# Kernel tuning notes

Measured on AMD Instinct MI355X. Metric: run time of the kernel, lower is better.

## Reference

```python
import jax, jax.numpy as jnp
import numpy as np
import math

B, CIN, CH, H, W = 4, 64, 32, 64, 64
M_CH, DEPTH, K = 4, 3, 8
NPF = CIN // 2  # num_pos_feats per axis; pos channels = 2*NPF = CIN
TEMPERATURE = 10000.0


def sine_pos(h, w, npf, temperature=TEMPERATURE):
    # PositionEmbeddingSine with normalize=False; cumsum of ones == arange(1, n+1)
    y_embed = jnp.arange(1, h + 1, dtype=jnp.float32)
    x_embed = jnp.arange(1, w + 1, dtype=jnp.float32)
    dim_t = jnp.arange(npf, dtype=jnp.float32)
    dim_t = temperature ** (2.0 * jnp.floor(dim_t / 2.0) / npf)
    pos_x = jnp.broadcast_to(x_embed[None, :, None] / dim_t, (h, w, npf))
    pos_y = jnp.broadcast_to(y_embed[:, None, None] / dim_t, (h, w, npf))

    def interleave(p):
        return jnp.stack([jnp.sin(p[..., 0::2]), jnp.cos(p[..., 1::2])], axis=-1).reshape(h, w, npf)

    pos = jnp.concatenate([interleave(pos_y), interleave(pos_x)], axis=-1)  # (h,w,2*npf)
    return jnp.transpose(pos, (2, 0, 1))  # (2*npf, h, w)


def conv2d(x, wgt, bias, pad):
    y = jax.lax.conv_general_dilated(
        x, wgt, window_strides=(1, 1), padding=[(pad, pad), (pad, pad)],
        dimension_numbers=('NCHW', 'OIHW', 'NCHW'))
    return y + bias[None, :, None, None]


def setup_inputs() -> dict:
    key = jax.random.key(0)
    ks = jax.random.split(key, 13)
    s = 0.05
    return {
        'f':    jax.random.normal(ks[0], (B, CH, H, W), jnp.float32),
        'map':  jax.random.normal(ks[1], (B, 1, 32, 32), jnp.float32),
        'f_q':  jax.random.normal(ks[2], (B, CIN, H, W), jnp.float32),
        'f_k':  jax.random.normal(ks[3], (B, CIN, H, W), jnp.float32),
        'm_k':  jax.random.normal(ks[4], (B, 1, 32, 32), jnp.float32),
        'wq':   jax.random.normal(ks[5], (M_CH, CIN), jnp.float32) * s,
        'wk':   jax.random.normal(ks[6], (M_CH, CIN), jnp.float32) * s,
        'w_in':  jax.random.normal(ks[7], (CH, CH, 1, 1), jnp.float32) * s,
        'b_in':  jax.random.normal(ks[8], (CH,), jnp.float32) * s,
        'w_mid': jax.random.normal(ks[9], (DEPTH, CH, CH, 3, 3), jnp.float32) * s,
        'b_mid': jax.random.normal(ks[10], (DEPTH, CH), jnp.float32) * s,
        'w_out': jax.random.normal(ks[11], (1, CH, 3, 3), jnp.float32) * s,
        'b_out': jax.random.normal(ks[12], (1,), jnp.float32) * s,
    }


def reference(f, map, f_q, f_k, m_k, wq, wk, w_in, b_in, w_mid, b_mid, w_out, b_out):
    b, c, h, w = f_q.shape
    hf, wf = f.shape[2], f.shape[3]
    # self.ret: bilinear resize to f's spatial size (align_corners=False)
    map_r = jax.image.resize(map, (b, 1, hf, wf), method='bilinear')
    m_k_r = jax.image.resize(m_k, (b, 1, hf, wf), method='bilinear')

    pos = sine_pos(h, w, NPF)[None]  # (1, CIN, h, w); same for pos_emb_h/pos_emb_l
    fq_emb = f_q + pos
    fk_emb = f_k + pos

    # 1x1 convs == channel matmuls
    query = jnp.einsum('mc,bchw->bhwm', wq, fq_emb).reshape(b, h * w, M_CH)  # (b, N, m)
    key_t = jnp.einsum('mc,bchw->bmhw', wk, fk_emb).reshape(b, M_CH, h * w)  # (b, m, N)

    sim = jnp.einsum('bqm,bmk->bqk', query, key_t)   # (b, N, N)
    sim = jax.nn.softmax(sim, axis=-2)                # softmax over query axis (dim=-2)

    value = (jnp.exp(m_k_r) / math.e).reshape(b, 1, h * w)  # broadcast over query axis
    context = sim * value
    context_k, _ = jax.lax.top_k(context, K)          # (b, N, K) over last (key) axis
    context_m = jnp.mean(context_k, axis=-1)          # (b, N)
    corrected_map = context_m.reshape(b, 1, h, w)

    corrected_map = corrected_map * map_r + map_r
    rmap = 1.0 - jax.nn.sigmoid(corrected_map)

    x = rmap * f  # broadcast over channel dim
    x = conv2d(x, w_in, b_in, 0)
    for i in range(DEPTH):
        x = jax.nn.relu(conv2d(x, w_mid[i], b_mid[i], 1))
    out = conv2d(x, w_out, b_out, 1) + corrected_map
    return (x, out, corrected_map)
```

## Files before the change

### kernel.cpp

```cpp
#include <hip/hip_runtime.h>
#include <hip/hip_bf16.h>
#include <math.h>

#define BB 4
#define CIN 64
#define CH 32
#define HH 64
#define WW 64
#define NN 4096
#define MCH 4
#define NQCH 32
#define LOG2E 1.4426950408889634f
#define L2_10K 13.287712379549449f

#define Q4_OFF     1024
#define K4_OFF     66560
#define CV_OFF     132096
#define RMAP_OFF   148480
#define CMAPF_OFF  164864
#define T8_OFF     181248
#define CPSUM_OFF  181248
#define XA_OFF     181248
#define XB_OFF     705536

#define OUT_X_OFF   0
#define OUT_O_OFF   524288
#define OUT_CM_OFF  540672

#define CE(x, y) { float ce_lo = fminf(x, y); y = fmaxf(x, y); x = ce_lo; }

__device__ __forceinline__ float bilin32(const float* src, int b, int y, int x) {
    float sy = 0.5f * y - 0.25f;
    float sx = 0.5f * x - 0.25f;
    float fy0 = floorf(sy), fx0 = floorf(sx);
    int y0 = (int)fy0, x0 = (int)fx0;
    float fy = sy - fy0, fx = sx - fx0;
    int y0c = min(max(y0, 0), 31), y1c = min(max(y0 + 1, 0), 31);
    int x0c = min(max(x0, 0), 31), x1c = min(max(x0 + 1, 0), 31);
    const float* p = src + b * 1024;
    float v00 = p[y0c * 32 + x0c], v01 = p[y0c * 32 + x1c];
    float v10 = p[y1c * 32 + x0c], v11 = p[y1c * 32 + x1c];
    float v0 = v00 + fx * (v01 - v00);
    float v1 = v10 + fx * (v11 - v10);
    return v0 + fy * (v1 - v0);
}

__global__ __launch_bounds__(512) void k1_qk(
        const float* __restrict__ fq, const float* __restrict__ fk,
        const float* __restrict__ wq, const float* __restrict__ wk,
        float* __restrict__ Q4, float* __restrict__ K4) {
    __shared__ float wqs[256], wks[256];
    __shared__ float pp[1024];
    __shared__ float red[512][9];
    int tid = threadIdx.x;
    if (tid < 256) { wqs[tid] = wq[tid]; wks[tid] = wk[tid]; }
    __syncthreads();

    if (tid < 64) {
        float coord = (float)(tid + 1);
        float qy[4] = {0,0,0,0}, qx[4] = {0,0,0,0}, ky[4] = {0,0,0,0}, kx[4] = {0,0,0,0};
        for (int c = 0; c < 32; ++c) {
            float e = (2.0f * (float)(c >> 1)) * (1.0f / 32.0f);
            float ang = coord * exp2f(-e * L2_10K);
            float pr = (c & 1) ? cosf(ang) : sinf(ang);
            #pragma unroll
            for (int m = 0; m < 4; ++m) {
                qy[m] += wqs[m * 64 + c] * pr;
                qx[m] += wqs[m * 64 + 32 + c] * pr;
                ky[m] += wks[m * 64 + c] * pr;
                kx[m] += wks[m * 64 + 32 + c] * pr;
            }
        }
        #pragma unroll
        for (int m = 0; m < 4; ++m) {
            pp[0 * 256 + m * 64 + tid] = qy[m];
            pp[1 * 256 + m * 64 + tid] = qx[m];
            pp[2 * 256 + m * 64 + tid] = ky[m];
            pp[3 * 256 + m * 64 + tid] = kx[m];
        }
    }

    int qi = tid & 63, g = tid >> 6;
    int gid = blockIdx.x * 64 + qi;
    int b = gid >> 12, hw = gid & 4095;
    const float* fqb = fq + (size_t)b * CIN * NN + hw;
    const float* fkb = fk + (size_t)b * CIN * NN + hw;
    float aq[4] = {0,0,0,0}, ak[4] = {0,0,0,0};
    int c0 = g * 8;
    #pragma unroll
    for (int c = c0; c < c0 + 8; ++c) {
        float vq = fqb[c * NN];
        float vk = fkb[c * NN];
        #pragma unroll
        for (int m = 0; m < 4; ++m) {
            aq[m] += wqs[m * 64 + c] * vq;
            ak[m] += wks[m * 64 + c] * vk;
        }
    }
    #pragma unroll
    for (int m = 0; m < 4; ++m) { red[tid][m] = aq[m]; red[tid][4 + m] = ak[m]; }
    __syncthreads();
    if (tid < 64) {
        int y = hw >> 6, x = hw & 63;
        float q4[4], k4[4];
        #pragma unroll
        for (int m = 0; m < 4; ++m) {
            float sq = 0.0f, sk = 0.0f;
            #pragma unroll
            for (int j = 0; j < 8; ++j) {
                sq += red[tid + 64 * j][m];
                sk += red[tid + 64 * j][4 + m];
            }
            q4[m] = LOG2E * (sq + pp[0 * 256 + m * 64 + y] + pp[1 * 256 + m * 64 + x]);
            k4[m] = sk + pp[2 * 256 + m * 64 + y] + pp[3 * 256 + m * 64 + x];
        }
        ((float4*)Q4)[gid] = make_float4(q4[0], q4[1], q4[2], q4[3]);
        ((float4*)K4)[gid] = make_float4(k4[0], k4[1], k4[2], k4[3]);
    }
}

__global__ void k2a_colstats(const float* __restrict__ Q4, const float* __restrict__ K4,
                             float* __restrict__ cpsum) {
    int blk = blockIdx.x;
    int kblk = blk & 7;   blk >>= 3;
    int qch  = blk & 31;  blk >>= 5;
    int b    = blk;
    int tid = threadIdx.x;
    const float4* Qg = (const float4*)Q4 + b * NN + qch * 128;
    int k0 = kblk * 512 + tid;
    float4 kva = ((const float4*)K4)[b * NN + k0];
    float4 kvb = ((const float4*)K4)[b * NN + k0 + 256];
    float sa = 0.0f, sb = 0.0f;
    #pragma unroll 8
    for (int i = 0; i < 128; ++i) {
        float4 q = Qg[i];
        float da = fmaf(q.x, kva.x, fmaf(q.y, kva.y, fmaf(q.z, kva.z, q.w * kva.w)));
        float db = fmaf(q.x, kvb.x, fmaf(q.y, kvb.y, fmaf(q.z, kvb.z, q.w * kvb.w)));
        sa += exp2f(da);
        sb += exp2f(db);
    }
    cpsum[(b * NQCH + qch) * NN + k0] = sa;
    cpsum[(b * NQCH + qch) * NN + k0 + 256] = sb;
}

__global__ void k2b_cmerge(const float* __restrict__ cpsum,
                           const float* __restrict__ m_k, float* __restrict__ cvals) {
    int gid = blockIdx.x * 256 + threadIdx.x;
    int b = gid >> 12, k = gid & 4095;
    float S = 0.0f;
    #pragma unroll
    for (int j = 0; j < NQCH; ++j) S += cpsum[(b * NQCH + j) * NN + k];
    float mk = bilin32(m_k, b, k >> 6, k & 63);
    cvals[gid] = LOG2E * (mk - 1.0f) - log2f(S);
}

__global__ __launch_bounds__(256) void k3a_scan(
        const float* __restrict__ Q4, const float* __restrict__ K4,
        const float* __restrict__ cvals, float* __restrict__ t8) {
    int blk = blockIdx.x;
    int kc = blk & 15;  blk >>= 4;
    int g4 = blk & 15;  blk >>= 4;
    int b  = blk;
    int tid = threadIdx.x;
    int wave = tid >> 6, lane = tid & 63;
    int qrow = (g4 * 4 + wave) * 64 + lane;
    float4 qv = ((const float4*)Q4)[b * NN + qrow];
    const float4* Kb = (const float4*)K4 + b * NN + kc * 256;
    const float* cb = cvals + b * NN + kc * 256;

    float t0=-1e30f,t1=-1e30f,t2=-1e30f,t3=-1e30f;
    float t4=-1e30f,t5=-1e30f,t6=-1e30f,t7=-1e30f;

    #pragma unroll 2
    for (int i0 = 0; i0 < 256; i0 += 8) {
        float4 k0 = Kb[i0 + 0]; float4 k1 = Kb[i0 + 1];
        float4 k2 = Kb[i0 + 2]; float4 k3 = Kb[i0 + 3];
        float4 k4 = Kb[i0 + 4]; float4 k5 = Kb[i0 + 5];
        float4 k6 = Kb[i0 + 6]; float4 k7 = Kb[i0 + 7];
        float s0 = fmaf(qv.x,k0.x, fmaf(qv.y,k0.y, fmaf(qv.z,k0.z, qv.w*k0.w))) + cb[i0+0];
        float s1 = fmaf(qv.x,k1.x, fmaf(qv.y,k1.y, fmaf(qv.z,k1.z, qv.w*k1.w))) + cb[i0+1];
        float s2 = fmaf(qv.x,k2.x, fmaf(qv.y,k2.y, fmaf(qv.z,k2.z, qv.w*k2.w))) + cb[i0+2];
        float s3 = fmaf(qv.x,k3.x, fmaf(qv.y,k3.y, fmaf(qv.z,k3.z, qv.w*k3.w))) + cb[i0+3];
        float s4 = fmaf(qv.x,k4.x, fmaf(qv.y,k4.y, fmaf(qv.z,k4.z, qv.w*k4.w))) + cb[i0+4];
        float s5 = fmaf(qv.x,k5.x, fmaf(qv.y,k5.y, fmaf(qv.z,k5.z, qv.w*k5.w))) + cb[i0+5];
        float s6 = fmaf(qv.x,k6.x, fmaf(qv.y,k6.y, fmaf(qv.z,k6.z, qv.w*k6.w))) + cb[i0+6];
        float s7 = fmaf(qv.x,k7.x, fmaf(qv.y,k7.y, fmaf(qv.z,k7.z, qv.w*k7.w))) + cb[i0+7];
        float bm = fmaxf(fmaxf(fmaxf(s0,s1), fmaxf(s2,s3)),
                         fmaxf(fmaxf(s4,s5), fmaxf(s6,s7)));
        if (bm > t0) {
            CE(s0,s1); CE(s2,s3); CE(s4,s5); CE(s6,s7);
            CE(s0,s2); CE(s1,s3); CE(s4,s6); CE(s5,s7);
            CE(s1,s2); CE(s5,s6);
            CE(s0,s4); CE(s1,s5); CE(s2,s6); CE(s3,s7);
            CE(s2,s4); CE(s3,s5);
            CE(s1,s2); CE(s3,s4); CE(s5,s6);
            t0 = fmaxf(t0, s7); t1 = fmaxf(t1, s6); t2 = fmaxf(t2, s5); t3 = fmaxf(t3, s4);
            t4 = fmaxf(t4, s3); t5 = fmaxf(t5, s2); t6 = fmaxf(t6, s1); t7 = fmaxf(t7, s0);
            CE(t0,t4); CE(t1,t5); CE(t2,t6); CE(t3,t7);
            CE(t0,t2); CE(t1,t3); CE(t4,t6); CE(t5,t7);
            CE(t0,t1); CE(t2,t3); CE(t4,t5); CE(t6,t7);
        }
    }
    float* o = t8 + ((size_t)(b * NN + qrow)) * 128 + kc * 8;
    o[0] = t0; o[1] = t1; o[2] = t2; o[3] = t3;
    o[4] = t4; o[5] = t5; o[6] = t6; o[7] = t7;
}

__global__ void k3b_merge(const float* __restrict__ t8, const float* __restrict__ mapin,
                          float* __restrict__ rmap, float* __restrict__ cmapf,
                          float* __restrict__ outp) {
    int tid = threadIdx.x;
    int qid = blockIdx.x * 4 + (tid >> 6);
    int lane = tid & 63;
    float va = t8[(size_t)qid * 128 + lane];
    float vb = t8[(size_t)qid * 128 + 64 + lane];
    float hi = fmaxf(va, vb), lo = fminf(va, vb);
    float sm = 0.0f;
    #pragma unroll
    for (int r = 0; r < 8; ++r) {
        float m = hi;
        int ln = lane;
        #pragma unroll
        for (int off = 32; off >= 1; off >>= 1) {
            float om = __shfl_xor(m, off);
            int ol = __shfl_xor(ln, off);
            if (om > m || (om == m && ol < ln)) { m = om; ln = ol; }
        }
        sm += exp2f(m);
        if (lane == ln) { hi = lo; lo = -1e30f; }
    }
    if (lane == 0) {
        float cmv = sm * 0.125f;
        int b = qid >> 12, hw = qid & 4095;
        float mr = bilin32(mapin, b, hw >> 6, hw & 63);
        float cm = cmv * mr + mr;
        float rm = 1.0f / (1.0f + __expf(cm));
        rmap[qid] = rm;
        cmapf[qid] = cm;
        outp[OUT_CM_OFF + qid] = cm;
    }
}

__global__ void k4_conv1(const float* __restrict__ f, const float* __restrict__ rmap,
                         const float* __restrict__ w_in, const float* __restrict__ b_in,
                         float* __restrict__ xout) {
    __shared__ float ws_[1024];
    __shared__ float bs[32];
    int tid = threadIdx.x;
    for (int i = tid; i < 1024; i += 256) ws_[i] = w_in[i];
    if (tid < 32) bs[tid] = b_in[tid];
    __syncthreads();
    int gid = blockIdx.x * 256 + tid;
    int hw = gid & 4095;
    int og = (gid >> 12) & 7;
    int b  = gid >> 15;
    float rm = rmap[b * NN + hw];
    float acc[4];
    #pragma unroll
    for (int j = 0; j < 4; ++j) acc[j] = bs[og * 4 + j];
    const float* fb = f + (size_t)b * CH * NN + hw;
    for (int i = 0; i < 32; ++i) {
        float v = fb[i * NN] * rm;
        #pragma unroll
        for (int j = 0; j < 4; ++j) acc[j] += ws_[(og * 4 + j) * 32 + i] * v;
    }
    float* xo = xout + (size_t)b * CH * NN + (og * 4) * NN + hw;
    #pragma unroll
    for (int j = 0; j < 4; ++j) xo[j * NN] = acc[j];
}

__global__ void k5_conv3(const float* __restrict__ xin, const float* __restrict__ w,
                         const float* __restrict__ bias, float* __restrict__ xout,
                         float* __restrict__ outx) {
    __shared__ float tile[32][324];
    __shared__ float wsm[1152];
    __shared__ float bsm[4];
    int blk = blockIdx.x;
    int og = blk & 7;  blk >>= 3;
    int tx = blk & 3;  blk >>= 2;
    int ty = blk & 3;  blk >>= 2;
    int b  = blk;
    int tid = threadIdx.x;
    for (int i = tid; i < 1152; i += 256) wsm[i] = w[og * 1152 + i];
    if (tid < 4) bsm[tid] = bias[og * 4 + tid];
    int y0 = ty * 16 - 1, x0 = tx * 16 - 1;
    for (int i = tid; i < 32 * 324; i += 256) {
        int c = i / 324, r = i % 324;
        int yy = r / 18, xx = r % 18;
        int gy = y0 + yy, gx = x0 + xx;
        float v = 0.0f;
        if (gy >= 0 && gy < 64 && gx >= 0 && gx < 64)
            v = xin[((size_t)b * CH + c) * NN + gy * 64 + gx];
        tile[c][r] = v;
    }
    __syncthreads();
    int py = tid >> 4, px = tid & 15;
    float acc[4];
    #pragma unroll
    for (int j = 0; j < 4; ++j) acc[j] = bsm[j];
    for (int i = 0; i < 32; ++i) {
        const float* tr = &tile[i][py * 18 + px];
        float v00 = tr[0],  v01 = tr[1],  v02 = tr[2];
        float v10 = tr[18], v11 = tr[19], v12 = tr[20];
        float v20 = tr[36], v21 = tr[37], v22 = tr[38];
        #pragma unroll
        for (int j = 0; j < 4; ++j) {
            const float* wj = &wsm[j * 288 + i * 9];
            acc[j] += v00 * wj[0] + v01 * wj[1] + v02 * wj[2]
                    + v10 * wj[3] + v11 * wj[4] + v12 * wj[5]
                    + v20 * wj[6] + v21 * wj[7] + v22 * wj[8];
        }
    }
    size_t base = (size_t)b * CH * NN + (size_t)(og * 4) * NN
                + (ty * 16 + py) * 64 + tx * 16 + px;
    #pragma unroll
    for (int j = 0; j < 4; ++j) {
        float r_ = fmaxf(acc[j], 0.0f);
        xout[base + j * NN] = r_;
        if (outx) outx[base + j * NN] = r_;
    }
}

__global__ void k6_convout(const float* __restrict__ xin, const float* __restrict__ w_out,
                           const float* __restrict__ b_out, const float* __restrict__ cmapf,
                           float* __restrict__ outp) {
    __shared__ float wsm[288];
    __shared__ float red[256];
    int tid = threadIdx.x;
    for (int i = tid; i < 288; i += 256) wsm[i] = w_out[i];
    int pxi = tid & 63, g = tid >> 6;
    int gid = blockIdx.x * 64 + pxi;
    int b = gid >> 12, hw = gid & 4095;
    int y = hw >> 6, x = hw & 63;
    __syncthreads();
    float acc = 0.0f;
    int c0 = g * 8;
    for (int i = c0; i < c0 + 8; ++i) {
        const float* xi = xin + ((size_t)b * CH + i) * NN;
        #pragma unroll
        for (int ky = 0; ky < 3; ++ky) {
            int gy = y + ky - 1;
            if (gy < 0 || gy > 63) continue;
            #pragma unroll
            for (int kx = 0; kx < 3; ++kx) {
                int gx = x + kx - 1;
                if (gx < 0 || gx > 63) continue;
                acc += xi[gy * 64 + gx] * wsm[i * 9 + ky * 3 + kx];
            }
        }
    }
    red[tid] = acc;
    __syncthreads();
    if (tid < 64) {
        float a = red[tid] + red[tid + 64] + red[tid + 128] + red[tid + 192]
                + b_out[0] + cmapf[gid];
        outp[OUT_O_OFF + gid] = a;
    }
}

extern "C" void kernel_launch(void* const* d_in, const int* in_sizes, int n_in,
                              void* d_out, int out_size, void* d_ws, size_t ws_size,
                              hipStream_t stream) {
    const float* f     = (const float*)d_in[0];
    const float* mapin = (const float*)d_in[1];
    const float* f_q   = (const float*)d_in[2];
    const float* f_k   = (const float*)d_in[3];
    const float* m_k   = (const float*)d_in[4];
    const float* wq    = (const float*)d_in[5];
    const float* wk    = (const float*)d_in[6];
    const float* w_in  = (const float*)d_in[7];
    const float* b_in  = (const float*)d_in[8];
    const float* w_mid = (const float*)d_in[9];
    const float* b_mid = (const float*)d_in[10];
    const float* w_out = (const float*)d_in[11];
    const float* b_out = (const float*)d_in[12];
    float* outp = (float*)d_out;
    float* ws = (float*)d_ws;

    float* Q4    = ws + Q4_OFF;
    float* K4    = ws + K4_OFF;
    float* CV    = ws + CV_OFF;
    float* CPSUM = ws + CPSUM_OFF;
    float* RMAP  = ws + RMAP_OFF;
    float* CMAPF = ws + CMAPF_OFF;
    float* T8    = ws + T8_OFF;
    float* XA    = ws + XA_OFF;
    float* XB    = ws + XB_OFF;

    k1_qk<<<256, 512, 0, stream>>>(f_q, f_k, wq, wk, Q4, K4);
    k2a_colstats<<<BB * NQCH * 8, 256, 0, stream>>>(Q4, K4, CPSUM);
    k2b_cmerge<<<64, 256, 0, stream>>>(CPSUM, m_k, CV);
    k3a_scan<<<BB * 16 * 16, 256, 0, stream>>>(Q4, K4, CV, T8);
    k3b_merge<<<BB * NN / 4, 256, 0, stream>>>(T8, mapin, RMAP, CMAPF, outp);
    k4_conv1<<<512, 256, 0, stream>>>(f, RMAP, w_in, b_in, XA);
    k5_conv3<<<512, 256, 0, stream>>>(XA, w_mid + 0 * 9216, b_mid + 0 * 32, XB, (float*)0);
    k5_conv3<<<512, 256, 0, stream>>>(XB, w_mid + 1 * 9216, b_mid + 1 * 32, XA, (float*)0);
    k5_conv3<<<512, 256, 0, stream>>>(XA, w_mid + 2 * 9216, b_mid + 2 * 32, XB, outp + OUT_X_OFF);
    k6_convout<<<256, 256, 0, stream>>>(XB, w_out, b_out, CMAPF, outp);
}
```

Before: 206.4 us.

## Double parallelism in qk projection, colstats and top-k scan kernels

Three attention kernels get finer work splits. k1 now processes 32 queries per block with 16 channel groups over 512 blocks. k2a gives each thread one key instead of two across twice as many blocks. k3a uses 512-thread blocks in which two wave groups each scan half of the 256-key chunk and merge their top-8 lists through shared memory. The aim is more waves in flight to hide latency on a GPU with many CUs, at the cost of extra reduction work, a block barrier and LDS traffic.

```diff
diff --git a/kernel.cpp b/kernel.cpp
--- a/kernel.cpp
+++ b/kernel.cpp
@@ -80,15 +80,15 @@
         }
     }
 
-    int qi = tid & 63, g = tid >> 6;
-    int gid = blockIdx.x * 64 + qi;
+    int qi = tid & 31, g = tid >> 5;
+    int gid = blockIdx.x * 32 + qi;
     int b = gid >> 12, hw = gid & 4095;
     const float* fqb = fq + (size_t)b * CIN * NN + hw;
     const float* fkb = fk + (size_t)b * CIN * NN + hw;
     float aq[4] = {0,0,0,0}, ak[4] = {0,0,0,0};
-    int c0 = g * 8;
-    #pragma unroll
-    for (int c = c0; c < c0 + 8; ++c) {
+    int c0 = g * 4;
+    #pragma unroll
+    for (int c = c0; c < c0 + 4; ++c) {
         float vq = fqb[c * NN];
         float vk = fkb[c * NN];
         #pragma unroll
@@ -100,16 +100,16 @@
     #pragma unroll
     for (int m = 0; m < 4; ++m) { red[tid][m] = aq[m]; red[tid][4 + m] = ak[m]; }
     __syncthreads();
-    if (tid < 64) {
+    if (tid < 32) {
         int y = hw >> 6, x = hw & 63;
         float q4[4], k4[4];
         #pragma unroll
         for (int m = 0; m < 4; ++m) {
             float sq = 0.0f, sk = 0.0f;
             #pragma unroll
-            for (int j = 0; j < 8; ++j) {
-                sq += red[tid + 64 * j][m];
-                sk += red[tid + 64 * j][4 + m];
+            for (int j = 0; j < 16; ++j) {
+                sq += red[tid + 32 * j][m];
+                sk += red[tid + 32 * j][4 + m];
             }
             q4[m] = LOG2E * (sq + pp[0 * 256 + m * 64 + y] + pp[1 * 256 + m * 64 + x]);
             k4[m] = sk + pp[2 * 256 + m * 64 + y] + pp[3 * 256 + m * 64 + x];
@@ -119,28 +119,25 @@
     }
 }
 
-__global__ void k2a_colstats(const float* __restrict__ Q4, const float* __restrict__ K4,
-                             float* __restrict__ cpsum) {
+__global__ __launch_bounds__(256) void k2a_colstats(
+        const float* __restrict__ Q4, const float* __restrict__ K4,
+        float* __restrict__ cpsum) {
     int blk = blockIdx.x;
-    int kblk = blk & 7;   blk >>= 3;
+    int kblk = blk & 15;  blk >>= 4;
     int qch  = blk & 31;  blk >>= 5;
     int b    = blk;
     int tid = threadIdx.x;
     const float4* Qg = (const float4*)Q4 + b * NN + qch * 128;
-    int k0 = kblk * 512 + tid;
-    float4 kva = ((const float4*)K4)[b * NN + k0];
-    float4 kvb = ((const float4*)K4)[b * NN + k0 + 256];
-    float sa = 0.0f, sb = 0.0f;
+    int k0 = kblk * 256 + tid;
+    float4 kv = ((const float4*)K4)[b * NN + k0];
+    float s = 0.0f;
     #pragma unroll 8
     for (int i = 0; i < 128; ++i) {
         float4 q = Qg[i];
-        float da = fmaf(q.x, kva.x, fmaf(q.y, kva.y, fmaf(q.z, kva.z, q.w * kva.w)));
-        float db = fmaf(q.x, kvb.x, fmaf(q.y, kvb.y, fmaf(q.z, kvb.z, q.w * kvb.w)));
-        sa += exp2f(da);
-        sb += exp2f(db);
-    }
-    cpsum[(b * NQCH + qch) * NN + k0] = sa;
-    cpsum[(b * NQCH + qch) * NN + k0 + 256] = sb;
+        float d = fmaf(q.x, kv.x, fmaf(q.y, kv.y, fmaf(q.z, kv.z, q.w * kv.w)));
+        s += exp2f(d);
+    }
+    cpsum[(b * NQCH + qch) * NN + k0] = s;
 }
 
 __global__ void k2b_cmerge(const float* __restrict__ cpsum,
@@ -154,25 +151,27 @@
     cvals[gid] = LOG2E * (mk - 1.0f) - log2f(S);
 }
 
-__global__ __launch_bounds__(256) void k3a_scan(
+__global__ __launch_bounds__(512) void k3a_scan(
         const float* __restrict__ Q4, const float* __restrict__ K4,
         const float* __restrict__ cvals, float* __restrict__ t8) {
+    __shared__ float sbuf[4][64][9];
     int blk = blockIdx.x;
     int kc = blk & 15;  blk >>= 4;
     int g4 = blk & 15;  blk >>= 4;
     int b  = blk;
     int tid = threadIdx.x;
     int wave = tid >> 6, lane = tid & 63;
-    int qrow = (g4 * 4 + wave) * 64 + lane;
+    int wsub = wave & 3, half = wave >> 2;
+    int qrow = (g4 * 4 + wsub) * 64 + lane;
     float4 qv = ((const float4*)Q4)[b * NN + qrow];
-    const float4* Kb = (const float4*)K4 + b * NN + kc * 256;
-    const float* cb = cvals + b * NN + kc * 256;
+    const float4* Kb = (const float4*)K4 + b * NN + kc * 256 + half * 128;
+    const float* cb = cvals + b * NN + kc * 256 + half * 128;
 
     float t0=-1e30f,t1=-1e30f,t2=-1e30f,t3=-1e30f;
     float t4=-1e30f,t5=-1e30f,t6=-1e30f,t7=-1e30f;
 
     #pragma unroll 2
-    for (int i0 = 0; i0 < 256; i0 += 8) {
+    for (int i0 = 0; i0 < 128; i0 += 8) {
         float4 k0 = Kb[i0 + 0]; float4 k1 = Kb[i0 + 1];
         float4 k2 = Kb[i0 + 2]; float4 k3 = Kb[i0 + 3];
         float4 k4 = Kb[i0 + 4]; float4 k5 = Kb[i0 + 5];
@@ -201,9 +200,26 @@
             CE(t0,t1); CE(t2,t3); CE(t4,t5); CE(t6,t7);
         }
     }
-    float* o = t8 + ((size_t)(b * NN + qrow)) * 128 + kc * 8;
-    o[0] = t0; o[1] = t1; o[2] = t2; o[3] = t3;
-    o[4] = t4; o[5] = t5; o[6] = t6; o[7] = t7;
+    if (half == 1) {
+        float* sb_ = &sbuf[wsub][lane][0];
+        sb_[0] = t0; sb_[1] = t1; sb_[2] = t2; sb_[3] = t3;
+        sb_[4] = t4; sb_[5] = t5; sb_[6] = t6; sb_[7] = t7;
+    }
+    __syncthreads();
+    if (half == 0) {
+        const float* sb_ = &sbuf[wsub][lane][0];
+        float f0 = fmaxf(t0, sb_[7]);
+        float f1 = fmaxf(t1, sb_[6]);
+        float f2 = fmaxf(t2, sb_[5]);
+        float f3 = fmaxf(t3, sb_[4]);
+        float f4 = fmaxf(t4, sb_[3]);
+        float f5 = fmaxf(t5, sb_[2]);
+        float f6 = fmaxf(t6, sb_[1]);
+        float f7 = fmaxf(t7, sb_[0]);
+        float* o = t8 + ((size_t)(b * NN + qrow)) * 128 + kc * 8;
+        o[0] = f0; o[1] = f1; o[2] = f2; o[3] = f3;
+        o[4] = f4; o[5] = f5; o[6] = f6; o[7] = f7;
+    }
 }
 
 __global__ void k3b_merge(const float* __restrict__ t8, const float* __restrict__ mapin,
@@ -387,10 +403,10 @@
     float* XA    = ws + XA_OFF;
     float* XB    = ws + XB_OFF;
 
-    k1_qk<<<256, 512, 0, stream>>>(f_q, f_k, wq, wk, Q4, K4);
-    k2a_colstats<<<BB * NQCH * 8, 256, 0, stream>>>(Q4, K4, CPSUM);
+    k1_qk<<<512, 512, 0, stream>>>(f_q, f_k, wq, wk, Q4, K4);
+    k2a_colstats<<<BB * NQCH * 16, 256, 0, stream>>>(Q4, K4, CPSUM);
     k2b_cmerge<<<64, 256, 0, stream>>>(CPSUM, m_k, CV);
-    k3a_scan<<<BB * 16 * 16, 256, 0, stream>>>(Q4, K4, CV, T8);
+    k3a_scan<<<BB * 16 * 16, 512, 0, stream>>>(Q4, K4, CV, T8);
     k3b_merge<<<BB * NN / 4, 256, 0, stream>>>(T8, mapin, RMAP, CMAPF, outp);
     k4_conv1<<<512, 256, 0, stream>>>(f, RMAP, w_in, b_in, XA);
     k5_conv3<<<512, 256, 0, stream>>>(XA, w_mid + 0 * 9216, b_mid + 0 * 32, XB, (float*)0);
```

Result: slower. 218.8 us (+6.0%).
